# Kernel tuning notes

Measured on AMD Instinct MI355X. Metric: run time of the kernel, lower is better.

The kernel has to match this reference:

```python
import jax, jax.numpy as jnp
import numpy as np
from jax import lax

HD = 768; HEADS = 16; DH = HD // HEADS
KS = ((8, 8, 8), (16, 4, 4), (4, 12, 12))
ST = ((16, 32, 32), (6, 32, 32), (16, 32, 32))
T_TOK = 833; SEQ = T_TOK + 1; GH = 32


def setup_inputs() -> dict:
    key = jax.random.key(0)
    keys = iter(jax.random.split(key, 64))
    def nrm(shape, s=0.02):
        return jax.random.normal(next(keys), shape, jnp.float32) * s
    d = {}
    d["x"] = nrm((8, 3, 64, 224, 224), 1.0)
    d["spa_feas"] = nrm((8, 200, 2048), 1.0)
    d["fea_len"] = jax.random.randint(next(keys), (8,), 1, 200, dtype=jnp.int32)
    d["pos_emb"] = nrm((1, SEQ, HD), 0.02)
    d["cls_tok"] = nrm((1, 1, HD), 0.02)
    d["conv_w"] = nrm((HD, 3) + KS[0], 1.0)  # torch .normal_() std=1
    d["conv_b"] = jnp.zeros((3, HD), jnp.float32)
    d["gn_g"] = jnp.ones((HD,), jnp.float32); d["gn_b"] = jnp.zeros((HD,), jnp.float32)
    d["pin_w"] = nrm((HD, HD)); d["pin_b"] = jnp.zeros((HD,), jnp.float32)
    for nm in ("ln1", "ln2", "ln3"):
        d[nm + "_g"] = jnp.ones((HD,), jnp.float32); d[nm + "_b"] = jnp.zeros((HD,), jnp.float32)
    for nm in ("a1", "a2"):
        d[nm + "_wq"] = nrm((HD, HD)); d[nm + "_wk"] = nrm((HD, HD)); d[nm + "_wv"] = nrm((HD, HD))
        d[nm + "_wo"] = nrm((HD, HD)); d[nm + "_bo"] = jnp.zeros((HD,), jnp.float32)
    d["ff_w1"] = nrm((4 * HD, HD, 9)); d["ff_b1"] = jnp.zeros((4 * HD,), jnp.float32)
    d["ff_w2"] = nrm((HD, 4 * HD, 9)); d["ff_b2"] = jnp.zeros((HD,), jnp.float32)
    d["pout_w"] = nrm((HD, HD)); d["pout_b"] = jnp.zeros((HD,), jnp.float32)  # zero_module'd in source; random for nontrivial test
    d["spa_w"] = nrm((HD, 2048)); d["spa_b"] = jnp.zeros((HD,), jnp.float32)
    d["gru_wih"] = nrm((3 * GH, HD)); d["gru_whh"] = nrm((3 * GH, GH))
    d["gru_bih"] = jnp.zeros((3 * GH,), jnp.float32); d["gru_bhh"] = jnp.zeros((3 * GH,), jnp.float32)
    d["qh_w"] = nrm((1, GH)); d["qh_b"] = jnp.zeros((1,), jnp.float32)
    return d


def _ln(x, g, b):
    m = x.mean(-1, keepdims=True)
    v = x.var(-1, keepdims=True)
    return (x - m) / jnp.sqrt(v + 1e-5) * g + b


def _gn(x, g, b):  # x: (b, c, t), 32 groups, eps=1e-6
    bn, c, t = x.shape
    xr = x.reshape(bn, 32, c // 32, t)
    m = xr.mean((2, 3), keepdims=True)
    v = xr.var((2, 3), keepdims=True)
    xr = ((xr - m) / jnp.sqrt(v + 1e-6)).reshape(bn, c, t)
    return xr * g[None, :, None] + b[None, :, None]


def _attn(x, wq, wk, wv, wo, bo):  # self-attention, hand-rolled like source
    b, n, _ = x.shape
    q = (x @ wq.T).reshape(b, n, HEADS, DH).transpose(0, 2, 1, 3)
    k = (x @ wk.T).reshape(b, n, HEADS, DH).transpose(0, 2, 1, 3)
    v = (x @ wv.T).reshape(b, n, HEADS, DH).transpose(0, 2, 1, 3)
    sim = jnp.einsum('bhid,bhjd->bhij', q, k) * (DH ** -0.5)
    attn = jax.nn.softmax(sim, axis=-1)
    o = jnp.einsum('bhij,bhjd->bhid', attn, v).transpose(0, 2, 1, 3).reshape(b, n, HD)
    return o @ wo.T + bo


def _conv1d(x, w, b, pad):  # x: (b, c, t)
    y = lax.conv_general_dilated(x, w, (1,), [(pad, pad)],
                                 dimension_numbers=('NCH', 'OIH', 'NCH'))
    return y + b[None, :, None]


def _tokenize(x, conv_w, conv_b):
    n = x.shape[0]
    tubes = []
    for i in range(3):
        if i == 0:
            w = conv_w
        else:
            # F.interpolate(..., mode='trilinear') (align_corners=False) == jax.image.resize trilinear
            w = jax.image.resize(conv_w, (HD, 3) + KS[i], method='trilinear')
        y = lax.conv_general_dilated(x, w, ST[i], 'VALID',
                                     dimension_numbers=('NCDHW', 'OIDHW', 'NCDHW'))
        y = y + conv_b[i][None, :, None, None, None]
        tubes.append(y.reshape(n, HD, -1))
    return jnp.concatenate(tubes, -1).transpose(0, 2, 1)  # (n, 833, 768)


def _forward(x, spa_feas, fea_len, pos_emb, cls_tok, conv_w, conv_b, gn_g, gn_b,
             pin_w, pin_b, ln1_g, ln1_b, ln2_g, ln2_b, ln3_g, ln3_b,
             a1_wq, a1_wk, a1_wv, a1_wo, a1_bo, a2_wq, a2_wk, a2_wv, a2_wo, a2_bo,
             ff_w1, ff_b1, ff_w2, ff_b2, pout_w, pout_b, spa_w, spa_b,
             gru_wih, gru_whh, gru_bih, gru_bhh, qh_w, qh_b):
    tok = _tokenize(x, conv_w, conv_b)                      # (n, 833, 768)
    n = tok.shape[0]
    h = jnp.concatenate([jnp.broadcast_to(cls_tok, (n, 1, HD)), tok], 1) + pos_emb
    # TemporalEncoder (depth 1, one layer)
    hc = h.transpose(0, 2, 1)                               # (n, c, t)
    x_in = hc
    z = _gn(hc, gn_g, gn_b)
    z = jnp.einsum('oc,bct->bot', pin_w, z) + pin_b[None, :, None]  # conv1d k=1
    z = z.transpose(0, 2, 1)                                # (n, t, c)
    # BasicTransformerBlock
    z = _attn(_ln(z, ln1_g, ln1_b), a1_wq, a1_wk, a1_wv, a1_wo, a1_bo) + z
    z = _attn(_ln(z, ln2_g, ln2_b), a2_wq, a2_wk, a2_wv, a2_wo, a2_bo) + z
    f = _ln(z, ln3_g, ln3_b).transpose(0, 2, 1)
    f = _conv1d(f, ff_w1, ff_b1, 4)
    f = jax.nn.gelu(f, approximate=False)
    f = _conv1d(f, ff_w2, ff_b2, 4)
    z = f.transpose(0, 2, 1) + z
    z = z.transpose(0, 2, 1)
    z = jnp.einsum('oc,bct->bot', pout_w, z) + pout_b[None, :, None]
    h = (z + x_in).transpose(0, 2, 1)                       # (n, 834, 768)
    spa = spa_feas @ spa_w.T + spa_b                        # (n, 200, 768)
    seq = jnp.concatenate([h, spa], 1)                      # (n, 1034, 768)
    # GRU (torch cell equations), batch_first
    gx = seq @ gru_wih.T + gru_bih                          # (n, T, 3*GH)
    h0 = jnp.zeros((n, GH), seq.dtype)
    def step(hp, gx_t):
        gh = hp @ gru_whh.T + gru_bhh
        r = jax.nn.sigmoid(gx_t[:, :GH] + gh[:, :GH])
        zg = jax.nn.sigmoid(gx_t[:, GH:2 * GH] + gh[:, GH:2 * GH])
        nn_ = jnp.tanh(gx_t[:, 2 * GH:] + r * gh[:, 2 * GH:])
        hn = (1 - zg) * nn_ + zg * hp
        return hn, hn
    _, outs = lax.scan(step, h0, gx.transpose(1, 0, 2))
    outs = outs.transpose(1, 0, 2)                          # (n, T, GH)
    q = outs @ qh_w.T + qh_b                                # (n, T, 1)
    L = fea_len.astype(q.dtype) + (T_TOK + 1)
    idx = jnp.arange(q.shape[1], dtype=q.dtype)
    mask = (idx[None, :] < L[:, None]).astype(q.dtype)
    return (q[..., 0] * mask).sum(1) / L                    # per-sample masked mean


def reference(x, spa_feas, fea_len, pos_emb, cls_tok, conv_w, conv_b, gn_g, gn_b,
              pin_w, pin_b, ln1_g, ln1_b, ln2_g, ln2_b, ln3_g, ln3_b,
              a1_wq, a1_wk, a1_wv, a1_wo, a1_bo, a2_wq, a2_wk, a2_wv, a2_wo, a2_bo,
              ff_w1, ff_b1, ff_w2, ff_b2, pout_w, pout_b, spa_w, spa_b,
              gru_wih, gru_whh, gru_bih, gru_bhh, qh_w, qh_b):
    return _forward(x, spa_feas, fea_len, pos_emb, cls_tok, conv_w, conv_b, gn_g, gn_b,
                    pin_w, pin_b, ln1_g, ln1_b, ln2_g, ln2_b, ln3_g, ln3_b,
                    a1_wq, a1_wk, a1_wv, a1_wo, a1_bo, a2_wq, a2_wk, a2_wv, a2_wo, a2_bo,
                    ff_w1, ff_b1, ff_w2, ff_b2, pout_w, pout_b, spa_w, spa_b,
                    gru_wih, gru_whh, gru_bih, gru_bhh, qh_w, qh_b)
```

## Files before the change

### kernel.cpp

```cpp
#include <hip/hip_runtime.h>


typedef short bf16x8 __attribute__((ext_vector_type(8)));
typedef float f32x4 __attribute__((ext_vector_type(4)));

__device__ __forceinline__ void split_bf16(float f, ushort& h, ushort& l) {
  uint u = __float_as_uint(f);
  uint rh = (u + 0x7FFFu + ((u >> 16) & 1u)) & 0xFFFF0000u;
  h = (ushort)(rh >> 16);
  float fl = f - __uint_as_float(rh);
  uint ul = __float_as_uint(fl);
  l = (ushort)((ul + 0x7FFFu + ((ul >> 16) & 1u)) >> 16);
}

__device__ __forceinline__ ushort bf16_rnd(float f) {
  uint u = __float_as_uint(f);
  return (ushort)((u + 0x7FFFu + ((u >> 16) & 1u)) >> 16);
}

__device__ __forceinline__ float gelu_exact(float v) {
  return 0.5f * v * (1.f + erff(v * 0.70710678118654752f));
}

__global__ void wsplit_kernel(const float* __restrict__ src, ushort* __restrict__ h,
                              ushort* __restrict__ l, int n4) {
  int i = blockIdx.x * 256 + threadIdx.x;
  if (i >= n4) return;
  float4 v = *(const float4*)(src + (size_t)i * 4);
  ushort hh[4], ll[4];
  split_bf16(v.x, hh[0], ll[0]);
  split_bf16(v.y, hh[1], ll[1]);
  split_bf16(v.z, hh[2], ll[2]);
  split_bf16(v.w, hh[3], ll[3]);
  *(ushort4*)(h + (size_t)i * 4) = make_ushort4(hh[0], hh[1], hh[2], hh[3]);
  *(ushort4*)(l + (size_t)i * 4) = make_ushort4(ll[0], ll[1], ll[2], ll[3]);
}

__device__ __forceinline__ void dim_weights(int j, int O, float* w) {
  float inv = 8.0f / (float)O;
  float ks  = inv > 1.0f ? inv : 1.0f;
  float sf  = ((float)j + 0.5f) * inv - 0.5f;
  float tot = 0.f;
#pragma unroll
  for (int i = 0; i < 8; i++) {
    float xx = fabsf(sf - (float)i) / ks;
    float t  = fmaxf(0.f, 1.f - xx);
    w[i] = t; tot += t;
  }
  float r = 1.f / tot;
#pragma unroll
  for (int i = 0; i < 8; i++) w[i] *= r;
}

__global__ void resize_w_split(const float* __restrict__ src, ushort* __restrict__ dh,
                               ushort* __restrict__ dl, int OD, int OH, int OW) {
  int idx = blockIdx.x * 256 + threadIdx.x;
  int tot = 2304 * OD * OH * OW;
  if (idx >= tot) return;
  int ow = idx % OW; int t = idx / OW;
  int oh = t % OH;   t /= OH;
  int od = t % OD;   int oc = t / OD;
  float wd[8], wh[8], ww[8];
  dim_weights(od, OD, wd);
  dim_weights(oh, OH, wh);
  dim_weights(ow, OW, ww);
  const float* s = src + (size_t)oc * 512;
  float acc = 0.f;
  for (int d = 0; d < 8; d++) {
    if (wd[d] == 0.f) continue;
    for (int h = 0; h < 8; h++) {
      if (wh[h] == 0.f) continue;
      float w2 = wd[d] * wh[h];
      for (int w = 0; w < 8; w++) {
        float w3 = w2 * ww[w];
        if (w3 != 0.f) acc += w3 * s[d * 64 + h * 8 + w];
      }
    }
  }
  ushort h2, l2;
  split_bf16(acc, h2, l2);
  dh[idx] = h2; dl[idx] = l2;
}

__global__ void im2col_split(const float* __restrict__ x, ushort* __restrict__ colh,
                             ushort* __restrict__ coll, int P, int K, int L,
                             int KD, int KH, int KW, int SD, int SH, int SW) {
  int idx = blockIdx.x * 256 + threadIdx.x;
  if (idx >= P * K) return;
  int p = idx / K;  int k = idx - p * K;
  int n = p / L;    int lp = p - n * L;
  int ld = lp / 49; int r = lp - ld * 49;
  int lh = r / 7;   int lw = r - lh * 7;
  int kvol = KD * KH * KW;
  int c = k / kvol; int r2 = k - c * kvol;
  int khw = KH * KW;
  int kd = r2 / khw; int r3 = r2 - kd * khw;
  int kh = r3 / KW;  int kw = r3 - kh * KW;
  int zd = ld * SD + kd, zh = lh * SH + kh, zw = lw * SW + kw;
  float v = x[((((size_t)n * 3 + c) * 64 + zd) * 224 + zh) * 224 + zw];
  ushort h, l;
  split_bf16(v, h, l);
  colh[(size_t)p * K + k] = h;
  coll[(size_t)p * K + k] = l;
}

template <int MODE>
__global__ __launch_bounds__(256) void gemm_bf3(
    const ushort* __restrict__ Ah, const ushort* __restrict__ Al,
    const ushort* __restrict__ Bh, const ushort* __restrict__ Bl,
    int M, int N, int K,
    const float* __restrict__ bias, const float* __restrict__ res, float scale,
    float* __restrict__ of, ushort* __restrict__ oh, ushort* __restrict__ ol,
    int mapL, int mapOff, int ldo) {
  __shared__ ushort ldsA[2 * 128 * 40];
  __shared__ ushort ldsB[2 * 128 * 40];
  const int tid = threadIdx.x;
  const int wave = tid >> 6, lane = tid & 63;
  const int lrow = lane & 15, kq = lane >> 4;
  const int i0 = blockIdx.y * 128;
  const int j0 = blockIdx.x * 128;
  const int wm = (wave & 1) * 64, wn = (wave >> 1) * 64;
  const int sr = tid >> 1, sp = tid & 1;

  f32x4 acc[4][4];
#pragma unroll
  for (int mi = 0; mi < 4; mi++)
#pragma unroll
    for (int ni = 0; ni < 4; ni++) acc[mi][ni] = (f32x4)0.f;

  for (int k0 = 0; k0 < K; k0 += 32) {
    __syncthreads();
    {
      uint4 d0 = make_uint4(0, 0, 0, 0), d1 = d0, d2 = d0, d3 = d0;
      if (i0 + sr < M) {
        const ushort* s = (sp ? Al : Ah) + (size_t)(i0 + sr) * K + k0;
        d0 = *(const uint4*)(const void*)s;
        d1 = *(const uint4*)(const void*)(s + 8);
        d2 = *(const uint4*)(const void*)(s + 16);
        d3 = *(const uint4*)(const void*)(s + 24);
      }
      ushort* dst = &ldsA[sp * 5120 + sr * 40];
      *(uint4*)(void*)dst = d0; *(uint4*)(void*)(dst + 8) = d1;
      *(uint4*)(void*)(dst + 16) = d2; *(uint4*)(void*)(dst + 24) = d3;
    }
    {
      uint4 d0 = make_uint4(0, 0, 0, 0), d1 = d0, d2 = d0, d3 = d0;
      if (j0 + sr < N) {
        const ushort* s = (sp ? Bl : Bh) + (size_t)(j0 + sr) * K + k0;
        d0 = *(const uint4*)(const void*)s;
        d1 = *(const uint4*)(const void*)(s + 8);
        d2 = *(const uint4*)(const void*)(s + 16);
        d3 = *(const uint4*)(const void*)(s + 24);
      }
      ushort* dst = &ldsB[sp * 5120 + sr * 40];
      *(uint4*)(void*)dst = d0; *(uint4*)(void*)(dst + 8) = d1;
      *(uint4*)(void*)(dst + 16) = d2; *(uint4*)(void*)(dst + 24) = d3;
    }
    __syncthreads();
    bf16x8 af[2][4], bf[2][4];
#pragma unroll
    for (int p = 0; p < 2; p++)
#pragma unroll
      for (int mi = 0; mi < 4; mi++)
        af[p][mi] = *(const bf16x8*)&ldsA[p * 5120 + (wm + mi * 16 + lrow) * 40 + kq * 8];
#pragma unroll
    for (int p = 0; p < 2; p++)
#pragma unroll
      for (int ni = 0; ni < 4; ni++)
        bf[p][ni] = *(const bf16x8*)&ldsB[p * 5120 + (wn + ni * 16 + lrow) * 40 + kq * 8];
#pragma unroll
    for (int mi = 0; mi < 4; mi++)
#pragma unroll
      for (int ni = 0; ni < 4; ni++)
        acc[mi][ni] = __builtin_amdgcn_mfma_f32_16x16x32_bf16(
            af[0][mi], bf[0][ni], acc[mi][ni], 0, 0, 0);
#pragma unroll
    for (int mi = 0; mi < 4; mi++)
#pragma unroll
      for (int ni = 0; ni < 4; ni++)
        acc[mi][ni] = __builtin_amdgcn_mfma_f32_16x16x32_bf16(
            af[0][mi], bf[1][ni], acc[mi][ni], 0, 0, 0);
#pragma unroll
    for (int mi = 0; mi < 4; mi++)
#pragma unroll
      for (int ni = 0; ni < 4; ni++)
        acc[mi][ni] = __builtin_amdgcn_mfma_f32_16x16x32_bf16(
            af[1][mi], bf[0][ni], acc[mi][ni], 0, 0, 0);
  }

#pragma unroll
  for (int mi = 0; mi < 4; mi++) {
#pragma unroll
    for (int r = 0; r < 4; r++) {
      int i = i0 + wm + mi * 16 + kq * 4 + r;
      if (i >= M) continue;
#pragma unroll
      for (int ni = 0; ni < 4; ni++) {
        int j = j0 + wn + ni * 16 + lrow;
        if (j >= N) continue;
        float v = acc[mi][ni][r];
        if (MODE == 0) {
          if (bias) v += bias[j];
          of[(size_t)i * ldo + j] = v;
        } else if (MODE == 1) {
          size_t oi = (size_t)i * 768 + j;
          of[oi] = v + bias[j] + res[oi];
        } else if (MODE == 2) {
          v *= scale;
          ushort h, l;
          split_bf16(v, h, l);
          size_t oi = (size_t)i * 768 + j;
          oh[oi] = h; ol[oi] = l;
        } else {
          int nn = i / mapL; int ll = i - nn * mapL;
          size_t oi = ((size_t)(nn * 1034 + mapOff + ll)) * 768 + j;
          v += bias[j];
          if (res) v += res[oi];
          of[oi] = v;
          if (oh) {
            ushort h, l;
            split_bf16(v, h, l);
            oh[oi] = h; ol[oi] = l;
          }
        }
      }
    }
  }
}

__global__ void wprep_kernel(const float* __restrict__ W, ushort* __restrict__ wh,
                             ushort* __restrict__ wl, int Jloc, int oOff,
                             int Cloc, int cOff, int Cfull) {
  size_t idx = (size_t)blockIdx.x * 256 + threadIdx.x;
  size_t tot = (size_t)9 * Jloc * Cloc;
  if (idx >= tot) return;
  int c = (int)(idx % Cloc);
  size_t t2 = idx / Cloc;
  int o = (int)(t2 % Jloc);
  int dt = (int)(t2 / Jloc);
  float f = W[((size_t)(oOff + o) * Cfull + (cOff + c)) * 9 + dt];
  ushort h, l;
  split_bf16(f, h, l);
  wh[idx] = h; wl[idx] = l;
}

__global__ __launch_bounds__(256) void ln_split_kernel(
    const float* __restrict__ in, const float* __restrict__ g,
    const float* __restrict__ b, ushort* __restrict__ oh, ushort* __restrict__ ol) {
  int row = blockIdx.x, tid = threadIdx.x;
  int n = row / 834, t = row - n * 834;
  const float* xp = in + (size_t)row * 768;
  float v0 = xp[tid], v1 = xp[tid + 256], v2 = xp[tid + 512];
  float s = v0 + v1 + v2;
  float sq = v0 * v0 + v1 * v1 + v2 * v2;
  __shared__ float red[8];
#pragma unroll
  for (int off = 32; off >= 1; off >>= 1) {
    s += __shfl_down(s, off, 64); sq += __shfl_down(sq, off, 64);
  }
  if ((tid & 63) == 0) { red[tid >> 6] = s; red[4 + (tid >> 6)] = sq; }
  __syncthreads();
  s = red[0] + red[1] + red[2] + red[3];
  sq = red[4] + red[5] + red[6] + red[7];
  float m = s * (1.f / 768.f);
  float var = sq * (1.f / 768.f) - m * m;
  float rs = rsqrtf(var + 1e-5f);
  size_t dbase = ((size_t)(n * 842 + 4 + t)) * 768;
  ushort h, l;
  float y0 = (v0 - m) * rs * g[tid] + b[tid];
  split_bf16(y0, h, l); oh[dbase + tid] = h; ol[dbase + tid] = l;
  float y1 = (v1 - m) * rs * g[tid + 256] + b[tid + 256];
  split_bf16(y1, h, l); oh[dbase + tid + 256] = h; ol[dbase + tid + 256] = l;
  float y2 = (v2 - m) * rs * g[tid + 512] + b[tid + 512];
  split_bf16(y2, h, l); oh[dbase + tid + 512] = h; ol[dbase + tid + 512] = l;
}

__global__ void pad_zero8(ushort* __restrict__ zh, ushort* __restrict__ zl,
                          ushort* __restrict__ fh, ushort* __restrict__ fl) {
  int idx = blockIdx.x * 256 + threadIdx.x;
  if (idx < 49152) {
    int c = idx % 768; int t2 = idx / 768;
    int rr = t2 & 7; int n = t2 >> 3;
    int row = (rr < 4) ? rr : (834 + rr);
    size_t d = ((size_t)(n * 842 + row)) * 768 + c;
    zh[d] = 0; zl[d] = 0;
  } else {
    int k = idx - 49152;
    if (k >= 196608) return;
    int c = k % 3072; int t2 = k / 3072;
    int rr = t2 & 7; int n = t2 >> 3;
    int row = (rr < 4) ? rr : (834 + rr);
    size_t d = ((size_t)(n * 842 + row)) * 3072 + c;
    fh[d] = 0; fl[d] = 0;
  }
}

template <int BN, int WM, int WN, int MODE>
__global__ __launch_bounds__(256) void conv_mfma(
    const ushort* __restrict__ Ah, const ushort* __restrict__ Al,
    const ushort* __restrict__ Wh, const ushort* __restrict__ Wl,
    int CinA, int cOff, int K, int J,
    const float* __restrict__ bias, int jOff,
    ushort* __restrict__ oh, ushort* __restrict__ ol,
    float* __restrict__ of) {
  constexpr int MI = WM / 16, NI = WN / 16;
  constexpr int BM = 2 * WM;
  constexpr int AR = BM + 8;
  __shared__ ushort ldsA[2 * AR * 40];
  __shared__ ushort ldsB[2 * BN * 40];
  const int tid = threadIdx.x;
  const int wave = tid >> 6, lane = tid & 63;
  const int lrow = lane & 15, kq = lane >> 4;
  const int t0 = blockIdx.x * BM;
  const int j0 = blockIdx.y * BN;
  const int bz = blockIdx.z;
  const int wm = (wave & 1) * WM;
  const int wn = (wave >> 1) * WN;

  f32x4 acc[MI][NI];
#pragma unroll
  for (int mi = 0; mi < MI; mi++)
#pragma unroll
    for (int ni = 0; ni < NI; ni++) acc[mi][ni] = (f32x4)0.f;

  for (int c0 = 0; c0 < K; c0 += 32) {
    __syncthreads();
    for (int task = tid; task < 4 * AR; task += 256) {
      int plane = task >= 2 * AR;
      int rem = task - plane * 2 * AR;
      int r = rem >> 1, h = rem & 1;
      const ushort* src = (plane ? Al : Ah) +
          ((size_t)(bz * 842 + t0 + r)) * CinA + cOff + c0 + h * 16;
      uint4 d0 = *(const uint4*)(const void*)src;
      uint4 d1 = *(const uint4*)(const void*)(src + 8);
      ushort* dst = &ldsA[plane * (AR * 40) + r * 40 + h * 16];
      *(uint4*)(void*)dst = d0;
      *(uint4*)(void*)(dst + 8) = d1;
    }
    for (int dt = 0; dt < 9; dt++) {
      if (dt > 0) __syncthreads();
      for (int task = tid; task < 4 * BN; task += 256) {
        int plane = task >= 2 * BN;
        int rem = task - plane * 2 * BN;
        int o = rem >> 1, h = rem & 1;
        const ushort* src = (plane ? Wl : Wh) +
            ((size_t)(dt * J + j0 + o)) * K + c0 + h * 16;
        uint4 d0 = *(const uint4*)(const void*)src;
        uint4 d1 = *(const uint4*)(const void*)(src + 8);
        ushort* dst = &ldsB[plane * (BN * 40) + o * 40 + h * 16];
        *(uint4*)(void*)dst = d0;
        *(uint4*)(void*)(dst + 8) = d1;
      }
      __syncthreads();
      bf16x8 af[2][MI], bf[2][NI];
#pragma unroll
      for (int p = 0; p < 2; p++)
#pragma unroll
        for (int mi = 0; mi < MI; mi++)
          af[p][mi] = *(const bf16x8*)&ldsA[p * (AR * 40) +
              (dt + wm + mi * 16 + lrow) * 40 + kq * 8];
#pragma unroll
      for (int p = 0; p < 2; p++)
#pragma unroll
        for (int ni = 0; ni < NI; ni++)
          bf[p][ni] = *(const bf16x8*)&ldsB[p * (BN * 40) +
              (wn + ni * 16 + lrow) * 40 + kq * 8];
#pragma unroll
      for (int mi = 0; mi < MI; mi++)
#pragma unroll
        for (int ni = 0; ni < NI; ni++)
          acc[mi][ni] = __builtin_amdgcn_mfma_f32_16x16x32_bf16(
              af[0][mi], bf[0][ni], acc[mi][ni], 0, 0, 0);
#pragma unroll
      for (int mi = 0; mi < MI; mi++)
#pragma unroll
        for (int ni = 0; ni < NI; ni++)
          acc[mi][ni] = __builtin_amdgcn_mfma_f32_16x16x32_bf16(
              af[0][mi], bf[1][ni], acc[mi][ni], 0, 0, 0);
#pragma unroll
      for (int mi = 0; mi < MI; mi++)
#pragma unroll
        for (int ni = 0; ni < NI; ni++)
          acc[mi][ni] = __builtin_amdgcn_mfma_f32_16x16x32_bf16(
              af[1][mi], bf[0][ni], acc[mi][ni], 0, 0, 0);
    }
  }

#pragma unroll
  for (int ni = 0; ni < NI; ni++) {
    int o = jOff + j0 + wn + ni * 16 + lrow;
    float bo = bias ? bias[o] : 0.f;
#pragma unroll
    for (int mi = 0; mi < MI; mi++) {
#pragma unroll
      for (int r = 0; r < 4; r++) {
        int t = t0 + wm + mi * 16 + kq * 4 + r;
        if (t < 834) {
          float v = acc[mi][ni][r] + bo;
          if (MODE == 1) {
            v = gelu_exact(v);
            ushort h, l;
            split_bf16(v, h, l);
            size_t d = ((size_t)(bz * 842 + 4 + t)) * 3072 + o;
            oh[d] = h; ol[d] = l;
          } else {
            size_t d = ((size_t)(bz * 834 + t)) * 768 + o;
            of[d] += v;
          }
        }
      }
    }
  }
}

__global__ void addpos_kernel(float* __restrict__ seq, const float* __restrict__ pos,
                              const float* __restrict__ cls) {
  int idx = blockIdx.x * 256 + threadIdx.x;
  if (idx >= 8 * 834 * 768) return;
  int c = idx % 768;
  int t = (idx / 768) % 834;
  int n = idx / (768 * 834);
  size_t off = ((size_t)(n * 1034 + t)) * 768 + c;
  float v = (t == 0) ? cls[c] : seq[off];
  seq[off] = v + pos[(size_t)t * 768 + c];
}

__global__ __launch_bounds__(256) void groupnorm_split(
    const float* __restrict__ seq, const float* __restrict__ g,
    const float* __restrict__ b, ushort* __restrict__ oh, ushort* __restrict__ ol) {
  int blk = blockIdx.x;
  int n = blk >> 5, grp = blk & 31;
  int tid = threadIdx.x;
  float s = 0.f, sq = 0.f;
  for (int e = tid; e < 20016; e += 256) {
    int t = e / 24; int cc = e - t * 24;
    float v = seq[((size_t)(n * 1034 + t)) * 768 + grp * 24 + cc];
    s += v; sq += v * v;
  }
  __shared__ float red[8];
#pragma unroll
  for (int off = 32; off >= 1; off >>= 1) {
    s += __shfl_down(s, off, 64); sq += __shfl_down(sq, off, 64);
  }
  if ((tid & 63) == 0) { red[tid >> 6] = s; red[4 + (tid >> 6)] = sq; }
  __syncthreads();
  s = red[0] + red[1] + red[2] + red[3];
  sq = red[4] + red[5] + red[6] + red[7];
  float m = s * (1.f / 20016.f);
  float var = sq * (1.f / 20016.f) - m * m;
  float rs = rsqrtf(var + 1e-6f);
  for (int e = tid; e < 20016; e += 256) {
    int t = e / 24; int cc = e - t * 24;
    int c = grp * 24 + cc;
    float v = seq[((size_t)(n * 1034 + t)) * 768 + c];
    float y = (v - m) * rs * g[c] + b[c];
    ushort h, l;
    split_bf16(y, h, l);
    size_t d = ((size_t)(n * 834 + t)) * 768 + c;
    oh[d] = h; ol[d] = l;
  }
}

__global__ __launch_bounds__(256) void ln_rows_split(
    const float* __restrict__ in, const float* __restrict__ g,
    const float* __restrict__ b, ushort* __restrict__ oh, ushort* __restrict__ ol) {
  int row = blockIdx.x, tid = threadIdx.x;
  const float* xp = in + (size_t)row * 768;
  float v0 = xp[tid], v1 = xp[tid + 256], v2 = xp[tid + 512];
  float s = v0 + v1 + v2;
  float sq = v0 * v0 + v1 * v1 + v2 * v2;
  __shared__ float red[8];
#pragma unroll
  for (int off = 32; off >= 1; off >>= 1) {
    s += __shfl_down(s, off, 64); sq += __shfl_down(sq, off, 64);
  }
  if ((tid & 63) == 0) { red[tid >> 6] = s; red[4 + (tid >> 6)] = sq; }
  __syncthreads();
  s = red[0] + red[1] + red[2] + red[3];
  sq = red[4] + red[5] + red[6] + red[7];
  float m = s * (1.f / 768.f);
  float var = sq * (1.f / 768.f) - m * m;
  float rs = rsqrtf(var + 1e-5f);
  size_t dbase = (size_t)row * 768;
  ushort h, l;
  float y0 = (v0 - m) * rs * g[tid] + b[tid];
  split_bf16(y0, h, l); oh[dbase + tid] = h; ol[dbase + tid] = l;
  float y1 = (v1 - m) * rs * g[tid + 256] + b[tid + 256];
  split_bf16(y1, h, l); oh[dbase + tid + 256] = h; ol[dbase + tid + 256] = l;
  float y2 = (v2 - m) * rs * g[tid + 512] + b[tid + 512];
  split_bf16(y2, h, l); oh[dbase + tid + 512] = h; ol[dbase + tid + 512] = l;
}

__global__ __launch_bounds__(256) void attn_mfma(
    const ushort* __restrict__ Qh, const ushort* __restrict__ Ql,
    const ushort* __restrict__ Kh, const ushort* __restrict__ Kl,
    const ushort* __restrict__ Vh, const ushort* __restrict__ Vl,
    ushort* __restrict__ Oh, ushort* __restrict__ Ol) {
  const int S = 834;
  __shared__ ushort sm[29952];
  ushort* Qs = sm;
  ushort* Ks = sm + 9216;
  ushort* Vt = sm + 18432;
  ushort* Ps = sm + 25344;
  const int tid = threadIdx.x;
  const int wave = tid >> 6, lane = tid & 63;
  const int lrow = lane & 15, kq = lane >> 4;
  const int qt = blockIdx.x, head = blockIdx.y, n = blockIdx.z;
  const size_t base = ((size_t)n * S) * 768 + head * 48;

  for (int e = tid; e < 18432; e += 256) sm[e] = 0;
  __syncthreads();
  if (tid < 128) {
    int r = tid >> 1, p = tid & 1;
    int q = qt * 64 + r;
    if (q < S) {
      const ushort* s = (p ? Ql : Qh) + base + (size_t)q * 768;
      ushort* d = &Qs[p * 4608 + r * 72];
#pragma unroll
      for (int seg = 0; seg < 6; seg++)
        *(uint4*)(void*)(d + seg * 8) = *(const uint4*)(const void*)(s + seg * 8);
    }
  }
  __syncthreads();

  bf16x8 aq[2][2];
#pragma unroll
  for (int p = 0; p < 2; p++)
#pragma unroll
    for (int c = 0; c < 2; c++)
      aq[p][c] = *(const bf16x8*)&Qs[p * 4608 + (wave * 16 + lrow) * 72 + c * 32 + kq * 8];

  float m4[4], l4[4];
  f32x4 accO[3];
#pragma unroll
  for (int r = 0; r < 4; r++) { m4[r] = -1e30f; l4[r] = 0.f; }
#pragma unroll
  for (int d = 0; d < 3; d++) accO[d] = (f32x4)0.f;

  for (int kt = 0; kt < S; kt += 64) {
    __syncthreads();
    if (tid < 128) {
      int r = tid >> 1, p = tid & 1;
      int ki = kt + r;
      if (ki < S) {
        const ushort* s = (p ? Kl : Kh) + base + (size_t)ki * 768;
        ushort* d = &Ks[p * 4608 + r * 72];
#pragma unroll
        for (int seg = 0; seg < 6; seg++)
          *(uint4*)(void*)(d + seg * 8) = *(const uint4*)(const void*)(s + seg * 8);
      }
    }
    for (int e = tid; e < 768; e += 256) {
      int p = e >= 384;
      int rem = e - p * 384;
      int kv = rem / 6, seg = rem - kv * 6;
      if (kt + kv < S) {
        uint4 d = *(const uint4*)(const void*)((p ? Vl : Vh) + base +
                                               (size_t)(kt + kv) * 768 + seg * 8);
        ushort* dst = &Vt[p * 3456 + kv];
        uint w[4] = {d.x, d.y, d.z, d.w};
#pragma unroll
        for (int u = 0; u < 4; u++) {
          dst[(seg * 8 + u * 2 + 0) * 72] = (ushort)(w[u] & 0xFFFFu);
          dst[(seg * 8 + u * 2 + 1) * 72] = (ushort)(w[u] >> 16);
        }
      }
    }
    __syncthreads();

    f32x4 s4[4];
#pragma unroll
    for (int ni = 0; ni < 4; ni++) s4[ni] = (f32x4)0.f;
#pragma unroll
    for (int ni = 0; ni < 4; ni++) {
      bf16x8 bk[2][2];
#pragma unroll
      for (int p = 0; p < 2; p++)
#pragma unroll
        for (int c = 0; c < 2; c++)
          bk[p][c] = *(const bf16x8*)&Ks[p * 4608 + (ni * 16 + lrow) * 72 + c * 32 + kq * 8];
#pragma unroll
      for (int c = 0; c < 2; c++)
        s4[ni] = __builtin_amdgcn_mfma_f32_16x16x32_bf16(aq[0][c], bk[0][c], s4[ni], 0, 0, 0);
#pragma unroll
      for (int c = 0; c < 2; c++)
        s4[ni] = __builtin_amdgcn_mfma_f32_16x16x32_bf16(aq[0][c], bk[1][c], s4[ni], 0, 0, 0);
#pragma unroll
      for (int c = 0; c < 2; c++)
        s4[ni] = __builtin_amdgcn_mfma_f32_16x16x32_bf16(aq[1][c], bk[0][c], s4[ni], 0, 0, 0);
    }

    bool valid[4];
#pragma unroll
    for (int ni = 0; ni < 4; ni++) valid[ni] = (kt + ni * 16 + lrow) < S;
    float pv[4][4];
#pragma unroll
    for (int r = 0; r < 4; r++) {
      float sv[4], mx = -1e30f;
#pragma unroll
      for (int ni = 0; ni < 4; ni++) {
        sv[ni] = valid[ni] ? s4[ni][r] : -1e30f;
        mx = fmaxf(mx, sv[ni]);
      }
#pragma unroll
      for (int off = 8; off >= 1; off >>= 1) mx = fmaxf(mx, __shfl_xor(mx, off, 64));
      float mnew = fmaxf(m4[r], mx);
      float al = __expf(m4[r] - mnew);
      float ps = 0.f;
#pragma unroll
      for (int ni = 0; ni < 4; ni++) {
        float p = valid[ni] ? __expf(sv[ni] - mnew) : 0.f;
        pv[ni][r] = p; ps += p;
      }
#pragma unroll
      for (int off = 8; off >= 1; off >>= 1) ps += __shfl_xor(ps, off, 64);
      l4[r] = l4[r] * al + ps;
      m4[r] = mnew;
#pragma unroll
      for (int d = 0; d < 3; d++) accO[d][r] *= al;
    }
#pragma unroll
    for (int ni = 0; ni < 4; ni++)
#pragma unroll
      for (int r = 0; r < 4; r++)
        Ps[(wave * 16 + kq * 4 + r) * 72 + ni * 16 + lrow] = bf16_rnd(pv[ni][r]);

    bf16x8 ap[2];
#pragma unroll
    for (int c = 0; c < 2; c++)
      ap[c] = *(const bf16x8*)&Ps[(wave * 16 + lrow) * 72 + c * 32 + kq * 8];
#pragma unroll
    for (int d = 0; d < 3; d++) {
      bf16x8 bv[2][2];
#pragma unroll
      for (int p = 0; p < 2; p++)
#pragma unroll
        for (int c = 0; c < 2; c++)
          bv[p][c] = *(const bf16x8*)&Vt[p * 3456 + (d * 16 + lrow) * 72 + c * 32 + kq * 8];
#pragma unroll
      for (int c = 0; c < 2; c++)
        accO[d] = __builtin_amdgcn_mfma_f32_16x16x32_bf16(ap[c], bv[0][c], accO[d], 0, 0, 0);
#pragma unroll
      for (int c = 0; c < 2; c++)
        accO[d] = __builtin_amdgcn_mfma_f32_16x16x32_bf16(ap[c], bv[1][c], accO[d], 0, 0, 0);
    }
  }

#pragma unroll
  for (int r = 0; r < 4; r++) {
    int q = qt * 64 + wave * 16 + kq * 4 + r;
    if (q >= S) continue;
    float inv = 1.f / l4[r];
#pragma unroll
    for (int d = 0; d < 3; d++) {
      float v = accO[d][r] * inv;
      ushort h, l;
      split_bf16(v, h, l);
      size_t oi = base + (size_t)q * 768 + d * 16 + lrow;
      Oh[oi] = h; Ol[oi] = l;
    }
  }
}

__global__ __launch_bounds__(64) void gru_kernel(
    const float* __restrict__ gx, const float* __restrict__ whh,
    const float* __restrict__ bhh, const float* __restrict__ qh_w,
    const float* __restrict__ qh_b, const int* __restrict__ fea_len,
    float* __restrict__ out) {
  int n = blockIdx.x;
  int lane = threadIdx.x;
  bool lo = lane < 32;
  float w1[32], w2[32];
#pragma unroll
  for (int i = 0; i < 32; i++) w1[i] = whh[lane * 32 + i];
#pragma unroll
  for (int i = 0; i < 32; i++) w2[i] = lo ? whh[(64 + lane) * 32 + i] : 0.f;
  float bh1 = bhh[lane];
  float bh2 = lo ? bhh[64 + lane] : 0.f;
  float qw  = lo ? qh_w[lane] : 0.f;
  float h_all[32];
#pragma unroll
  for (int i = 0; i < 32; i++) h_all[i] = 0.f;
  float hown = 0.f, acc = 0.f;
  int L = fea_len[n] + 834;
  const float* gb = gx + (size_t)n * 1034 * 96;
  for (int t = 0; t < 1034; t++) {
    if (t >= L) break;
    const float* g = gb + (size_t)t * 96;
    float g1 = g[lane];
    float g2 = lo ? g[64 + lane] : 0.f;
    float gh1 = bh1, gh2 = bh2;
#pragma unroll
    for (int i = 0; i < 32; i++) {
      gh1 = fmaf(h_all[i], w1[i], gh1);
      gh2 = fmaf(h_all[i], w2[i], gh2);
    }
    float s1 = g1 + gh1;
    float szg = __shfl(s1, (lane + 32) & 63, 64);
    float rg = 1.f / (1.f + expf(-s1));
    float zg = 1.f / (1.f + expf(-szg));
    float nn = tanhf(fmaf(rg, gh2, g2));
    float hn = (1.f - zg) * nn + zg * hown;
    if (lo) { hown = hn; acc = fmaf(hn, qw, acc); }
#pragma unroll
    for (int i = 0; i < 32; i++) h_all[i] = __shfl(hn, i, 64);
  }
#pragma unroll
  for (int off = 16; off >= 1; off >>= 1) acc += __shfl_down(acc, off, 64);
  if (lane == 0) out[n] = acc / (float)L + qh_b[0];
}

extern "C" void kernel_launch(void* const* d_in, const int* in_sizes, int n_in,
                              void* d_out, int out_size, void* d_ws, size_t ws_size,
                              hipStream_t stream) {
  const float* x        = (const float*)d_in[0];
  const float* spa_feas = (const float*)d_in[1];
  const int*   fea_len  = (const int*)d_in[2];
  const float* pos_emb  = (const float*)d_in[3];
  const float* cls_tok  = (const float*)d_in[4];
  const float* conv_w   = (const float*)d_in[5];
  const float* conv_b   = (const float*)d_in[6];
  const float* gn_g     = (const float*)d_in[7];
  const float* gn_b     = (const float*)d_in[8];
  const float* pin_w    = (const float*)d_in[9];
  const float* pin_b    = (const float*)d_in[10];
  const float* ln_g[3]  = {(const float*)d_in[11], (const float*)d_in[13], (const float*)d_in[15]};
  const float* ln_b[3]  = {(const float*)d_in[12], (const float*)d_in[14], (const float*)d_in[16]};
  const float* wq[2] = {(const float*)d_in[17], (const float*)d_in[22]};
  const float* wk[2] = {(const float*)d_in[18], (const float*)d_in[23]};
  const float* wv[2] = {(const float*)d_in[19], (const float*)d_in[24]};
  const float* wo[2] = {(const float*)d_in[20], (const float*)d_in[25]};
  const float* bo[2] = {(const float*)d_in[21], (const float*)d_in[26]};
  const float* ff_w1 = (const float*)d_in[27];
  const float* ff_b1 = (const float*)d_in[28];
  const float* ff_w2 = (const float*)d_in[29];
  const float* ff_b2 = (const float*)d_in[30];
  const float* pout_w = (const float*)d_in[31];
  const float* pout_b = (const float*)d_in[32];
  const float* spa_w  = (const float*)d_in[33];
  const float* spa_b  = (const float*)d_in[34];
  const float* gru_wih = (const float*)d_in[35];
  const float* gru_whh = (const float*)d_in[36];
  const float* gru_bih = (const float*)d_in[37];
  const float* gru_bhh = (const float*)d_in[38];
  const float* qh_w = (const float*)d_in[39];
  const float* qh_b = (const float*)d_in[40];
  float* outp = (float*)d_out;

  float* ws  = (float*)d_ws;
  float* seq = ws;
  float* z   = seq + 6352896;
  ushort* R  = (ushort*)(ws + 11476992);

  size_t co = 0;
  ushort* pinH = R + co; co += 589824; ushort* pinL = R + co; co += 589824;
  ushort *wqH[2], *wqL[2], *wkH[2], *wkL[2], *wvH[2], *wvL[2], *woH[2], *woL[2];
  for (int l = 0; l < 2; l++) {
    wqH[l] = R + co; co += 589824; wqL[l] = R + co; co += 589824;
    wkH[l] = R + co; co += 589824; wkL[l] = R + co; co += 589824;
    wvH[l] = R + co; co += 589824; wvL[l] = R + co; co += 589824;
    woH[l] = R + co; co += 589824; woL[l] = R + co; co += 589824;
  }
  ushort* aPh = R + co; co += 5124096; ushort* aPl = R + co; co += 5124096;
  ushort* QPh = R + co; co += 5124096; ushort* QPl = R + co; co += 5124096;
  ushort* KPh = R + co; co += 5124096; ushort* KPl = R + co; co += 5124096;
  ushort* VPh = R + co; co += 5124096; ushort* VPl = R + co; co += 5124096;
  ushort* oPh = R + co; co += 5124096; ushort* oPl = R + co; co += 5124096;
  ushort* colH = R + co; co += 2709504; ushort* colL = R + co; co += 2709504;
  ushort* cwH  = R + co; co += 1179648; ushort* cwL  = R + co; co += 1179648;
  ushort* w1rH = R + co; co += 589824;  ushort* w1rL = R + co; co += 589824;
  ushort* w2rH = R + co; co += 1327104; ushort* w2rL = R + co; co += 1327104;

  ushort* fmH  = R;                ushort* fmL  = R + 20692992;
  ushort* zsH  = R + 41385984;     ushort* zsL  = R + 46559232;
  ushort* ffwH = R + 51732480;     ushort* ffwL = R + 62349312;
  ushort* zPh = R + 40992768;     ushort* zPl = R + 46116864;
  ushort* poutH = R + 51240960;   ushort* poutL = R + 51830784;
  ushort* spaWH = R + 52420608;   ushort* spaWL = R + 53993472;
  ushort* wihH = R + 55566336;    ushort* wihL = R + 55640064;
  ushort* spaInH = R + 55713792;  ushort* spaInL = R + 58990592;
  ushort* seqPh = R;              ushort* seqPl = R + 6352896;
  float* gx = (float*)(R + 12705792);

  const float QSCALE = 0.14433756729740644f;

  resize_w_split<<<2304, 256, 0, stream>>>(conv_w, w1rH, w1rL, 16, 4, 4);
  resize_w_split<<<5184, 256, 0, stream>>>(conv_w, w2rH, w2rL, 4, 12, 12);
  wsplit_kernel<<<1152, 256, 0, stream>>>(conv_w, cwH, cwL, 294912);
  im2col_split<<<9408, 256, 0, stream>>>(x, colH, colL, 1568, 1536, 196, 8, 8, 8, 16, 32, 32);
  gemm_bf3<3><<<dim3(6, 13), 256, 0, stream>>>(colH, colL, cwH, cwL, 1568, 768, 1536,
      conv_b, nullptr, 1.f, seq, nullptr, nullptr, 196, 1, 768);
  im2col_split<<<10584, 256, 0, stream>>>(x, colH, colL, 3528, 768, 441, 16, 4, 4, 6, 32, 32);
  gemm_bf3<3><<<dim3(6, 28), 256, 0, stream>>>(colH, colL, w1rH, w1rL, 3528, 768, 768,
      conv_b + 768, nullptr, 1.f, seq, nullptr, nullptr, 441, 197, 768);
  im2col_split<<<10584, 256, 0, stream>>>(x, colH, colL, 1568, 1728, 196, 4, 12, 12, 16, 32, 32);
  gemm_bf3<3><<<dim3(6, 13), 256, 0, stream>>>(colH, colL, w2rH, w2rL, 1568, 768, 1728,
      conv_b + 1536, nullptr, 1.f, seq, nullptr, nullptr, 196, 638, 768);
  addpos_kernel<<<20016, 256, 0, stream>>>(seq, pos_emb, cls_tok);

  wsplit_kernel<<<576, 256, 0, stream>>>(pin_w, pinH, pinL, 147456);
  for (int l = 0; l < 2; l++) {
    wsplit_kernel<<<576, 256, 0, stream>>>(wq[l], wqH[l], wqL[l], 147456);
    wsplit_kernel<<<576, 256, 0, stream>>>(wk[l], wkH[l], wkL[l], 147456);
    wsplit_kernel<<<576, 256, 0, stream>>>(wv[l], wvH[l], wvL[l], 147456);
    wsplit_kernel<<<576, 256, 0, stream>>>(wo[l], woH[l], woL[l], 147456);
  }

  groupnorm_split<<<256, 256, 0, stream>>>(seq, gn_g, gn_b, aPh, aPl);
  gemm_bf3<0><<<dim3(6, 53), 256, 0, stream>>>(aPh, aPl, pinH, pinL, 6672, 768, 768,
      pin_b, nullptr, 1.f, z, nullptr, nullptr, 0, 0, 768);

  for (int l = 0; l < 2; l++) {
    ln_rows_split<<<6672, 256, 0, stream>>>(z, ln_g[l], ln_b[l], aPh, aPl);
    gemm_bf3<2><<<dim3(6, 53), 256, 0, stream>>>(aPh, aPl, wqH[l], wqL[l], 6672, 768, 768,
        nullptr, nullptr, QSCALE, nullptr, QPh, QPl, 0, 0, 768);
    gemm_bf3<2><<<dim3(6, 53), 256, 0, stream>>>(aPh, aPl, wkH[l], wkL[l], 6672, 768, 768,
        nullptr, nullptr, 1.f, nullptr, KPh, KPl, 0, 0, 768);
    gemm_bf3<2><<<dim3(6, 53), 256, 0, stream>>>(aPh, aPl, wvH[l], wvL[l], 6672, 768, 768,
        nullptr, nullptr, 1.f, nullptr, VPh, VPl, 0, 0, 768);
    attn_mfma<<<dim3(14, 16, 8), 256, 0, stream>>>(QPh, QPl, KPh, KPl, VPh, VPl, oPh, oPl);
    gemm_bf3<1><<<dim3(6, 53), 256, 0, stream>>>(oPh, oPl, woH[l], woL[l], 6672, 768, 768,
        bo[l], z, 1.f, z, nullptr, nullptr, 0, 0, 768);
  }

  ln_split_kernel<<<6672, 256, 0, stream>>>(z, ln_g[2], ln_b[2], zsH, zsL);
  pad_zero8<<<960, 256, 0, stream>>>(zsH, zsL, fmH, fmL);
  for (int jh = 0; jh < 2; jh++) {
    wprep_kernel<<<41472, 256, 0, stream>>>(ff_w1, ffwH, ffwL, 1536, jh * 1536, 768, 0, 768);
    conv_mfma<64, 64, 32, 1><<<dim3(7, 24, 8), 256, 0, stream>>>(
        zsH, zsL, ffwH, ffwL, 768, 0, 768, 1536, ff_b1, jh * 1536, fmH, fmL, nullptr);
  }
  for (int kh = 0; kh < 2; kh++) {
    wprep_kernel<<<41472, 256, 0, stream>>>(ff_w2, ffwH, ffwL, 768, 0, 1536, kh * 1536, 3072);
    conv_mfma<64, 32, 32, 2><<<dim3(14, 12, 8), 256, 0, stream>>>(
        fmH, fmL, ffwH, ffwL, 3072, kh * 1536, 1536, 768,
        (kh == 1) ? ff_b2 : nullptr, 0, nullptr, nullptr, z);
  }

  wsplit_kernel<<<5005, 256, 0, stream>>>(z, zPh, zPl, 1281024);
  wsplit_kernel<<<576, 256, 0, stream>>>(pout_w, poutH, poutL, 147456);
  wsplit_kernel<<<1536, 256, 0, stream>>>(spa_w, spaWH, spaWL, 393216);
  wsplit_kernel<<<72, 256, 0, stream>>>(gru_wih, wihH, wihL, 18432);
  wsplit_kernel<<<3200, 256, 0, stream>>>(spa_feas, spaInH, spaInL, 819200);
  gemm_bf3<3><<<dim3(6, 53), 256, 0, stream>>>(zPh, zPl, poutH, poutL, 6672, 768, 768,
      pout_b, seq, 1.f, seq, seqPh, seqPl, 834, 0, 768);
  gemm_bf3<3><<<dim3(6, 13), 256, 0, stream>>>(spaInH, spaInL, spaWH, spaWL, 1600, 768, 2048,
      spa_b, nullptr, 1.f, seq, seqPh, seqPl, 200, 834, 768);
  gemm_bf3<0><<<dim3(1, 65), 256, 0, stream>>>(seqPh, seqPl, wihH, wihL, 8272, 96, 768,
      gru_bih, nullptr, 1.f, gx, nullptr, nullptr, 0, 0, 96);
  gru_kernel<<<8, 64, 0, stream>>>(gx, gru_whh, gru_bhh, qh_w, qh_b, fea_len, outp);
}
```

Baseline: 6.244 ms.

## Use 128x128 conv tiles with 64x64 per-wave subtiles and batch-interleaved 1D grid

Replaces the templated conv_mfma tile shapes (64-wide N, 32-64 row waves) with a fixed 128x128 block tile where each of four waves computes a 64x64 subtile. The launch becomes a 1D grid with the batch index in the low bits, so neighbouring blocks share the same weight tile. This raises MFMA work per LDS load and cuts redundant weight fetches. The cost is more accumulator registers (64 floats x4), larger LDS, and fewer blocks (672 and 336), which may lower occupancy and leave CUs idle.

```diff
diff --git a/kernel.cpp b/kernel.cpp
--- a/kernel.cpp
+++ b/kernel.cpp
@@ -295,103 +295,103 @@
   }
 }
 
-template <int BN, int WM, int WN, int MODE>
+template <int MODE>
 __global__ __launch_bounds__(256) void conv_mfma(
     const ushort* __restrict__ Ah, const ushort* __restrict__ Al,
     const ushort* __restrict__ Wh, const ushort* __restrict__ Wl,
     int CinA, int cOff, int K, int J,
     const float* __restrict__ bias, int jOff,
     ushort* __restrict__ oh, ushort* __restrict__ ol,
-    float* __restrict__ of) {
-  constexpr int MI = WM / 16, NI = WN / 16;
-  constexpr int BM = 2 * WM;
-  constexpr int AR = BM + 8;
+    float* __restrict__ of, int nT) {
+  constexpr int AR = 136;
   __shared__ ushort ldsA[2 * AR * 40];
-  __shared__ ushort ldsB[2 * BN * 40];
+  __shared__ ushort ldsB[2 * 128 * 40];
   const int tid = threadIdx.x;
   const int wave = tid >> 6, lane = tid & 63;
   const int lrow = lane & 15, kq = lane >> 4;
-  const int t0 = blockIdx.x * BM;
-  const int j0 = blockIdx.y * BN;
-  const int bz = blockIdx.z;
-  const int wm = (wave & 1) * WM;
-  const int wn = (wave >> 1) * WN;
-
-  f32x4 acc[MI][NI];
-#pragma unroll
-  for (int mi = 0; mi < MI; mi++)
-#pragma unroll
-    for (int ni = 0; ni < NI; ni++) acc[mi][ni] = (f32x4)0.f;
+  const int b = blockIdx.x;
+  const int bz = b & 7;
+  const int r0 = b >> 3;
+  const int t0 = (r0 % nT) * 128;
+  const int j0 = (r0 / nT) * 128;
+  const int wm = (wave & 1) * 64;
+  const int wn = (wave >> 1) * 64;
+
+  f32x4 acc[4][4];
+#pragma unroll
+  for (int mi = 0; mi < 4; mi++)
+#pragma unroll
+    for (int ni = 0; ni < 4; ni++) acc[mi][ni] = (f32x4)0.f;
 
   for (int c0 = 0; c0 < K; c0 += 32) {
     __syncthreads();
     for (int task = tid; task < 4 * AR; task += 256) {
       int plane = task >= 2 * AR;
       int rem = task - plane * 2 * AR;
-      int r = rem >> 1, h = rem & 1;
+      int rr = rem >> 1, h = rem & 1;
       const ushort* src = (plane ? Al : Ah) +
-          ((size_t)(bz * 842 + t0 + r)) * CinA + cOff + c0 + h * 16;
+          ((size_t)(bz * 842 + t0 + rr)) * CinA + cOff + c0 + h * 16;
       uint4 d0 = *(const uint4*)(const void*)src;
       uint4 d1 = *(const uint4*)(const void*)(src + 8);
-      ushort* dst = &ldsA[plane * (AR * 40) + r * 40 + h * 16];
+      ushort* dst = &ldsA[plane * (AR * 40) + rr * 40 + h * 16];
       *(uint4*)(void*)dst = d0;
       *(uint4*)(void*)(dst + 8) = d1;
     }
     for (int dt = 0; dt < 9; dt++) {
       if (dt > 0) __syncthreads();
-      for (int task = tid; task < 4 * BN; task += 256) {
-        int plane = task >= 2 * BN;
-        int rem = task - plane * 2 * BN;
+      for (int task = tid; task < 512; task += 256) {
+        int plane = task >= 256;
+        int rem = task - plane * 256;
         int o = rem >> 1, h = rem & 1;
         const ushort* src = (plane ? Wl : Wh) +
             ((size_t)(dt * J + j0 + o)) * K + c0 + h * 16;
         uint4 d0 = *(const uint4*)(const void*)src;
         uint4 d1 = *(const uint4*)(const void*)(src + 8);
-        ushort* dst = &ldsB[plane * (BN * 40) + o * 40 + h * 16];
+        ushort* dst = &ldsB[plane * 5120 + o * 40 + h * 16];
         *(uint4*)(void*)dst = d0;
         *(uint4*)(void*)(dst + 8) = d1;
       }
       __syncthreads();
-      bf16x8 af[2][MI], bf[2][NI];
+      bf16x8 af[2][4], bf[2][4];
 #pragma unroll
       for (int p = 0; p < 2; p++)
 #pragma unroll
-        for (int mi = 0; mi < MI; mi++)
+        for (int mi = 0; mi < 4; mi++)
           af[p][mi] = *(const bf16x8*)&ldsA[p * (AR * 40) +
               (dt + wm + mi * 16 + lrow) * 40 + kq * 8];
 #pragma unroll
       for (int p = 0; p < 2; p++)
 #pragma unroll
-        for (int ni = 0; ni < NI; ni++)
-          bf[p][ni] = *(const bf16x8*)&ldsB[p * (BN * 40) +
+        for (int ni = 0; ni < 4; ni++)
+          bf[p][ni] = *(const bf16x8*)&ldsB[p * 5120 +
               (wn + ni * 16 + lrow) * 40 + kq * 8];
 #pragma unroll
-      for (int mi = 0; mi < MI; mi++)
-#pragma unroll
-        for (int ni = 0; ni < NI; ni++)
+      for (int mi = 0; mi < 4; mi++)
+#pragma unroll
+        for (int ni = 0; ni < 4; ni++)
           acc[mi][ni] = __builtin_amdgcn_mfma_f32_16x16x32_bf16(
               af[0][mi], bf[0][ni], acc[mi][ni], 0, 0, 0);
 #pragma unroll
-      for (int mi = 0; mi < MI; mi++)
-#pragma unroll
-        for (int ni = 0; ni < NI; ni++)
+      for (int mi = 0; mi < 4; mi++)
+#pragma unroll
+        for (int ni = 0; ni < 4; ni++)
           acc[mi][ni] = __builtin_amdgcn_mfma_f32_16x16x32_bf16(
               af[0][mi], bf[1][ni], acc[mi][ni], 0, 0, 0);
 #pragma unroll
-      for (int mi = 0; mi < MI; mi++)
-#pragma unroll
-        for (int ni = 0; ni < NI; ni++)
+      for (int mi = 0; mi < 4; mi++)
+#pragma unroll
+        for (int ni = 0; ni < 4; ni++)
           acc[mi][ni] = __builtin_amdgcn_mfma_f32_16x16x32_bf16(
               af[1][mi], bf[0][ni], acc[mi][ni], 0, 0, 0);
     }
   }
 
 #pragma unroll
-  for (int ni = 0; ni < NI; ni++) {
+  for (int ni = 0; ni < 4; ni++) {
     int o = jOff + j0 + wn + ni * 16 + lrow;
     float bo = bias ? bias[o] : 0.f;
 #pragma unroll
-    for (int mi = 0; mi < MI; mi++) {
+    for (int mi = 0; mi < 4; mi++) {
 #pragma unroll
       for (int r = 0; r < 4; r++) {
         int t = t0 + wm + mi * 16 + kq * 4 + r;
@@ -827,14 +827,14 @@
   pad_zero8<<<960, 256, 0, stream>>>(zsH, zsL, fmH, fmL);
   for (int jh = 0; jh < 2; jh++) {
     wprep_kernel<<<41472, 256, 0, stream>>>(ff_w1, ffwH, ffwL, 1536, jh * 1536, 768, 0, 768);
-    conv_mfma<64, 64, 32, 1><<<dim3(7, 24, 8), 256, 0, stream>>>(
-        zsH, zsL, ffwH, ffwL, 768, 0, 768, 1536, ff_b1, jh * 1536, fmH, fmL, nullptr);
+    conv_mfma<1><<<8 * 7 * 12, 256, 0, stream>>>(
+        zsH, zsL, ffwH, ffwL, 768, 0, 768, 1536, ff_b1, jh * 1536, fmH, fmL, nullptr, 7);
   }
   for (int kh = 0; kh < 2; kh++) {
     wprep_kernel<<<41472, 256, 0, stream>>>(ff_w2, ffwH, ffwL, 768, 0, 1536, kh * 1536, 3072);
-    conv_mfma<64, 32, 32, 2><<<dim3(14, 12, 8), 256, 0, stream>>>(
+    conv_mfma<2><<<8 * 7 * 6, 256, 0, stream>>>(
         fmH, fmL, ffwH, ffwL, 3072, kh * 1536, 1536, 768,
-        (kh == 1) ? ff_b2 : nullptr, 0, nullptr, nullptr, z);
+        (kh == 1) ? ff_b2 : nullptr, 0, nullptr, nullptr, z, 7);
   }
 
   wsplit_kernel<<<5005, 256, 0, stream>>>(z, zPh, zPl, 1281024);
```

Result: faster. 5.668 ms (-9.2%).
